# Kernel tuning notes

Measured on AMD Instinct MI355X. Metric: run time of the kernel, lower is better.

The kernel has to match this reference:

```python
import jax, jax.numpy as jnp
import numpy as np

N_NODES = 80000
N_EDGES = 1280000
D_NODE = 128
D_EDGE = 32
D_HID = 64
NEG_SLOPE = 0.2


def setup_inputs() -> dict:
    key = jax.random.key(0)
    ks = jax.random.split(key, 9)
    return {
        "node_features": jax.random.normal(ks[0], (N_NODES, D_NODE), dtype=jnp.float32),
        "edge_features": jax.random.normal(ks[1], (N_EDGES, D_EDGE), dtype=jnp.float32),
        "edge_index": jax.random.randint(ks[2], (2, N_EDGES), 0, N_NODES, dtype=jnp.int64),
        # params: w (node Linear), edgew (edge Linear), attn (3*hid -> 1)
        "w_w": jax.random.normal(ks[3], (D_NODE, D_HID), dtype=jnp.float32) / np.sqrt(D_NODE),
        "w_b": jax.random.normal(ks[4], (D_HID,), dtype=jnp.float32) * 0.01,
        "ew_w": jax.random.normal(ks[5], (D_EDGE, D_HID), dtype=jnp.float32) / np.sqrt(D_EDGE),
        "ew_b": jax.random.normal(ks[6], (D_HID,), dtype=jnp.float32) * 0.01,
        "a_w": jax.random.normal(ks[7], (3 * D_HID, 1), dtype=jnp.float32) / np.sqrt(3 * D_HID),
        "a_b": jax.random.normal(ks[8], (1,), dtype=jnp.float32) * 0.01,
    }


def reference(node_features, edge_features, edge_index, w_w, w_b, ew_w, ew_b, a_w, a_b):
    n_nodes = node_features.shape[0]
    h = node_features @ w_w + w_b              # [N, H]
    edge_h = edge_features @ ew_w + ew_b       # [E, H]
    tgt = edge_index[0]                        # target (softmax group) nodes i
    nbr = edge_index[1]                        # neighbor nodes j
    h_i = h[tgt]                               # [E, H] gather
    h_j = h[nbr]                               # [E, H] gather
    h_concat = jnp.concatenate([h_i, h_j, edge_h], axis=-1)  # [E, 3H]
    eij = jax.nn.leaky_relu(h_concat @ a_w + a_b, negative_slope=NEG_SLOPE)  # [E, 1]
    # scatter-softmax over edges grouped by target node (numerically stable)
    seg_max = jax.ops.segment_max(eij, tgt, num_segments=n_nodes)            # [N, 1]
    ex = jnp.exp(eij - seg_max[tgt])
    seg_sum = jax.ops.segment_sum(ex, tgt, num_segments=n_nodes)             # [N, 1]
    alpha = ex / seg_sum[tgt]                                                # [E, 1]
    # (dropout omitted for deterministic reference)
    message = alpha * h_j                                                    # [E, H]
    out = jax.ops.segment_sum(message, tgt, num_segments=n_nodes)            # [N, H]
    return jax.nn.elu(out)
```

## Files before the change

kernel.cpp:

```cpp
#include <hip/hip_runtime.h>
#include <math.h>

#define N_NODES 80000
#define N_EDGES 1280000
#define D_NODE  128
#define D_EDGE  32
#define D_HID   64
#define NEG_SLOPE 0.2f
#define NB 313
#define CAP 4608
#define EB_BLK 512
#define EB_CHUNK 2048
#define EB_NCHUNK (N_EDGES / EB_CHUNK)

__device__ inline float waveReduceSum(float v) {
    #pragma unroll
    for (int o = 32; o > 0; o >>= 1) v += __shfl_xor(v, o);
    return v;
}
__device__ inline unsigned short f2bf(float f) {
    unsigned u = __float_as_uint(f);
    return (unsigned short)((u + 0x7FFF + ((u >> 16) & 1)) >> 16);
}
__device__ inline float bf2f(unsigned short v) {
    return __uint_as_float(((unsigned)v) << 16);
}

__global__ __launch_bounds__(256) void node_kernel(
        const float* __restrict__ nf, const float* __restrict__ w_w,
        const float* __restrict__ w_b, const float* __restrict__ a_w,
        unsigned short* __restrict__ hb, float* __restrict__ s1, float* __restrict__ s2) {
    __shared__ float Ws[D_HID * D_NODE];
    __shared__ float Xs[32][D_NODE];
    for (int i = threadIdx.x; i < D_NODE * D_HID; i += 256) {
        int k = i >> 6, d = i & 63;
        Ws[d * D_NODE + (((k >> 2) ^ (d & 7)) << 2) + (k & 3)] = w_w[i];
    }
    int lane = threadIdx.x & 63;
    int wv   = threadIdx.x >> 6;
    float wb = w_b[lane];
    float a1 = a_w[lane];
    float a2 = a_w[D_HID + lane];
    const float* wrow = &Ws[lane * D_NODE];
    const int nTiles = N_NODES / 32;
    for (int tile = blockIdx.x; tile < nTiles; tile += gridDim.x) {
        int n0 = tile * 32;
        __syncthreads();
        {
            const float4* src = (const float4*)(nf + (size_t)n0 * D_NODE);
            float4* dst = (float4*)&Xs[0][0];
            #pragma unroll
            for (int j = 0; j < 4; ++j)
                dst[threadIdx.x + 256 * j] = src[threadIdx.x + 256 * j];
        }
        __syncthreads();
        float acc[8] = {0.f, 0.f, 0.f, 0.f, 0.f, 0.f, 0.f, 0.f};
        const float* xs = &Xs[wv * 8][0];
        #pragma unroll 4
        for (int k4 = 0; k4 < 32; ++k4) {
            float4 w = *(const float4*)&wrow[(k4 ^ (lane & 7)) << 2];
            #pragma unroll
            for (int n = 0; n < 8; ++n) {
                float4 x = *(const float4*)&xs[n * D_NODE + (k4 << 2)];
                acc[n] += w.x * x.x + w.y * x.y + w.z * x.z + w.w * x.w;
            }
        }
        #pragma unroll
        for (int n = 0; n < 8; ++n) {
            int node = n0 + wv * 8 + n;
            float hv = acc[n] + wb;
            hb[(size_t)node * D_HID + lane] = f2bf(hv);
            float r1 = waveReduceSum(hv * a1);
            float r2 = waveReduceSum(hv * a2);
            if (lane == 0) { s1[node] = r1; s2[node] = r2; }
        }
    }
}

__global__ __launch_bounds__(EB_BLK) void edge_bin_kernel(
        const float* __restrict__ ef, const int* __restrict__ eidx,
        const float* __restrict__ s2v,
        const float* __restrict__ ew_w, const float* __restrict__ ew_b,
        const float* __restrict__ a_w, const float* __restrict__ a_b,
        int* __restrict__ bcnt, int2* __restrict__ binned) {
    __shared__ float cs[D_EDGE];
    __shared__ float bes;
    __shared__ int hist[NB], gbase[NB], rank[NB];
    __shared__ float sq [EB_CHUNK];
    __shared__ int   stg[EB_CHUNK];
    __shared__ int   snb[EB_CHUNK];
    int tid = threadIdx.x;
    if (tid < D_EDGE) {
        float s = 0.f;
        #pragma unroll
        for (int d = 0; d < D_HID; ++d) s += ew_w[tid * D_HID + d] * a_w[2 * D_HID + d];
        cs[tid] = s;
    } else if (tid == D_EDGE) {
        float s = 0.f;
        #pragma unroll
        for (int d = 0; d < D_HID; ++d) s += ew_b[d] * a_w[2 * D_HID + d];
        bes = s + a_b[0];
    }
    int qd = tid >> 2;
    int j  = tid & 3;
    for (int c = blockIdx.x; c < EB_NCHUNK; c += gridDim.x) {
        for (int i = tid; i < NB; i += EB_BLK) { hist[i] = 0; rank[i] = 0; }
        __syncthreads();
        int e0 = c * EB_CHUNK;
        #pragma unroll
        for (int k = 0; k < 4; ++k) {
            int idx = k * EB_BLK + tid;
            int e = e0 + idx;
            int tg = eidx[e];
            int nb = eidx[N_EDGES + e];
            stg[idx] = tg;
            snb[idx] = nb;
            sq [idx] = bes + s2v[nb];
            atomicAdd(&hist[tg >> 8], 1);
        }
        __syncthreads();
        #pragma unroll 2
        for (int rr = 0; rr < EB_CHUNK / 128; ++rr) {
            int idx = rr * 128 + qd;
            int e = e0 + idx;
            const float4* f4 = (const float4*)ef;
            float4 fa = f4[(size_t)e * 8 + j];
            float4 fb = f4[(size_t)e * 8 + 4 + j];
            const float4 c1 = *(const float4*)&cs[j * 4];
            const float4 c2 = *(const float4*)&cs[16 + j * 4];
            float p = fa.x * c1.x + fa.y * c1.y + fa.z * c1.z + fa.w * c1.w
                    + fb.x * c2.x + fb.y * c2.y + fb.z * c2.z + fb.w * c2.w;
            p += __shfl_xor(p, 1);
            p += __shfl_xor(p, 2);
            if (j == 0) sq[idx] += p;
        }
        __syncthreads();
        for (int i = tid; i < NB; i += EB_BLK) {
            int cc = hist[i];
            if (cc) gbase[i] = i * CAP + atomicAdd(&bcnt[i], cc);
        }
        __syncthreads();
        #pragma unroll
        for (int k = 0; k < 4; ++k) {
            int idx = k * EB_BLK + tid;
            int tg = stg[idx];
            int b  = tg >> 8;
            int r  = atomicAdd(&rank[b], 1);
            binned[gbase[b] + r] = make_int2(((tg & 255) << 17) | snb[idx],
                                             __float_as_int(sq[idx]));
        }
        __syncthreads();
    }
}

__global__ __launch_bounds__(512) void bucket_scan_kernel(
        const int* __restrict__ bcnt, int* __restrict__ bbase,
        int* __restrict__ node_off) {
    __shared__ int buf[512];
    int v = (threadIdx.x < NB) ? bcnt[threadIdx.x] : 0;
    buf[threadIdx.x] = v;
    __syncthreads();
    for (int ofs = 1; ofs < 512; ofs <<= 1) {
        int t = (threadIdx.x >= (unsigned)ofs) ? buf[threadIdx.x - ofs] : 0;
        __syncthreads();
        buf[threadIdx.x] += t;
        __syncthreads();
    }
    if (threadIdx.x < NB) bbase[threadIdx.x] = buf[threadIdx.x] - v;
    if (threadIdx.x == NB - 1) bbase[NB] = buf[threadIdx.x];
    if (threadIdx.x == 0) node_off[N_NODES] = N_EDGES;
}

__global__ __launch_bounds__(256) void bucket_csr_kernel(
        const int* __restrict__ bcnt, const int* __restrict__ bbase,
        const int2* __restrict__ binned, int* __restrict__ node_off,
        int2* __restrict__ pay2) {
    __shared__ int nhist[256], buf[256], ncur[256];
    int b = blockIdx.x;
    int in0  = b * CAP;
    int cnt  = bcnt[b];
    int out0 = bbase[b];
    nhist[threadIdx.x] = 0;
    __syncthreads();
    for (int i = threadIdx.x; i < cnt; i += 256)
        atomicAdd(&nhist[binned[in0 + i].x >> 17], 1);
    __syncthreads();
    int v = nhist[threadIdx.x];
    buf[threadIdx.x] = v;
    __syncthreads();
    for (int ofs = 1; ofs < 256; ofs <<= 1) {
        int t = (threadIdx.x >= (unsigned)ofs) ? buf[threadIdx.x - ofs] : 0;
        __syncthreads();
        buf[threadIdx.x] += t;
        __syncthreads();
    }
    int excl = buf[threadIdx.x] - v;
    int n = b * 256 + (int)threadIdx.x;
    if (n < N_NODES) node_off[n] = out0 + excl;
    ncur[threadIdx.x] = excl;
    __syncthreads();
    for (int i = threadIdx.x; i < cnt; i += 256) {
        int2 p = binned[in0 + i];
        int r = atomicAdd(&ncur[p.x >> 17], 1);
        pay2[out0 + r] = make_int2(p.x & 0x1FFFF, p.y);
    }
}

__global__ __launch_bounds__(256) void accum_kernel(
        const int* __restrict__ node_off, const int2* __restrict__ pay2,
        const float* __restrict__ s1, const unsigned short* __restrict__ hb,
        float* __restrict__ out) {
    __shared__ float exs[4][64];
    __shared__ int   nbs[4][64];
    int wv = threadIdx.x >> 6, lane = threadIdx.x & 63;
    int node = blockIdx.x * 4 + wv;
    if (node >= N_NODES) return;
    int base = node_off[node];
    int cnt  = node_off[node + 1] - base;
    if (cnt == 0) { out[(size_t)node * D_HID + lane] = 0.f; return; }
    float s1i = s1[node];
    float sumex = 0.f, acc = 0.f;
    for (int c0 = 0; c0 < cnt; c0 += 64) {
        int i = c0 + lane;
        int nc = min(64, cnt - c0);
        float exv = 0.f; int nb = 0;
        if (i < cnt) {
            int2 p = pay2[base + i];
            nb = p.x;
            float s = s1i + __int_as_float(p.y);
            s = (s > 0.f) ? s : NEG_SLOPE * s;
            exv = __expf(s);
        }
        sumex += exv;
        exs[wv][lane] = exv;
        nbs[wv][lane] = nb;
        for (int j = 0; j < nc; ++j) {
            acc += exs[wv][j] * bf2f(hb[(size_t)nbs[wv][j] * D_HID + lane]);
        }
    }
    sumex = waveReduceSum(sumex);
    float o = acc / sumex;
    out[(size_t)node * D_HID + lane] = (o > 0.f) ? o : (__expf(o) - 1.f);
}

extern "C" void kernel_launch(void* const* d_in, const int* in_sizes, int n_in,
                              void* d_out, int out_size, void* d_ws, size_t ws_size,
                              hipStream_t stream) {
    const float* nf   = (const float*)d_in[0];
    const float* ef   = (const float*)d_in[1];
    const int*   eidx = (const int*)d_in[2];
    const float* w_w  = (const float*)d_in[3];
    const float* w_b  = (const float*)d_in[4];
    const float* ew_w = (const float*)d_in[5];
    const float* ew_b = (const float*)d_in[6];
    const float* a_w  = (const float*)d_in[7];
    const float* a_b  = (const float*)d_in[8];
    float* out = (float*)d_out;

    char* ws = (char*)d_ws;
    size_t o = 0;
    auto alloc = [&](size_t bytes) -> void* {
        void* p = ws + o;
        o = (o + bytes + 255) & ~(size_t)255;
        return p;
    };
    unsigned short* hb  = (unsigned short*)alloc((size_t)N_NODES * D_HID * 2);
    float* s1       = (float*)alloc((size_t)N_NODES * 4);
    float* s2       = (float*)alloc((size_t)N_NODES * 4);
    int*   bcnt     = (int*)alloc((size_t)NB * 4);
    int*   bbase    = (int*)alloc((size_t)(NB + 1) * 4);
    int*   node_off = (int*)alloc((size_t)(N_NODES + 1) * 4);
    int2*  binned   = (int2*)alloc((size_t)NB * CAP * 8);
    int2*  pay2     = (int2*)alloc((size_t)N_EDGES * 8);

    hipMemsetAsync(bcnt, 0, (size_t)NB * 4, stream);

    node_kernel<<<1250, 256, 0, stream>>>(nf, w_w, w_b, a_w, hb, s1, s2);
    edge_bin_kernel<<<EB_NCHUNK, EB_BLK, 0, stream>>>(ef, eidx, s2, ew_w, ew_b, a_w, a_b, bcnt, binned);
    bucket_scan_kernel<<<1, 512, 0, stream>>>(bcnt, bbase, node_off);
    bucket_csr_kernel<<<NB, 256, 0, stream>>>(bcnt, bbase, binned, node_off, pay2);
    accum_kernel<<<(N_NODES + 3) / 4, 256, 0, stream>>>(node_off, pay2, s1, hb, out);
}
```

Measured before the change: 163.5 us.

## Pad bucket counters, shrink edge-bin blocks, and pair-vectorize bf16 gathers in accum

Pads the global per-bucket atomic counters to a 16-int stride so they no longer share cache lines under contention. The edge binning kernel now runs one 1024-edge chunk per 256-thread block with no grid-stride loop, and hoists the coefficient loads out of the loop. The accumulation kernel has each lane load two bf16 values as one 32-bit word, with the two half-waves handling alternate edges and combined by a shuffle, then writes float2 outputs. This cuts the number of gather instructions and raises occupancy, at the cost of more blocks and atomics and an extra cross-half reduction.

```diff
diff --git a/kernel.cpp b/kernel.cpp
--- a/kernel.cpp
+++ b/kernel.cpp
@@ -9,8 +9,9 @@
 #define NEG_SLOPE 0.2f
 #define NB 313
 #define CAP 4608
-#define EB_BLK 512
-#define EB_CHUNK 2048
+#define BCNT_STRIDE 16
+#define EB_BLK 256
+#define EB_CHUNK 1024
 #define EB_NCHUNK (N_EDGES / EB_CHUNK)
 
 __device__ inline float waveReduceSum(float v) {
@@ -101,55 +102,53 @@
         for (int d = 0; d < D_HID; ++d) s += ew_b[d] * a_w[2 * D_HID + d];
         bes = s + a_b[0];
     }
+    for (int i = tid; i < NB; i += EB_BLK) { hist[i] = 0; rank[i] = 0; }
+    __syncthreads();
+    int c = blockIdx.x;
+    int e0 = c * EB_CHUNK;
+    #pragma unroll
+    for (int k = 0; k < 4; ++k) {
+        int idx = k * EB_BLK + tid;
+        int e = e0 + idx;
+        int tg = eidx[e];
+        int nb = eidx[N_EDGES + e];
+        stg[idx] = tg;
+        snb[idx] = nb;
+        sq [idx] = bes + s2v[nb];
+        atomicAdd(&hist[tg >> 8], 1);
+    }
+    __syncthreads();
     int qd = tid >> 2;
     int j  = tid & 3;
-    for (int c = blockIdx.x; c < EB_NCHUNK; c += gridDim.x) {
-        for (int i = tid; i < NB; i += EB_BLK) { hist[i] = 0; rank[i] = 0; }
-        __syncthreads();
-        int e0 = c * EB_CHUNK;
-        #pragma unroll
-        for (int k = 0; k < 4; ++k) {
-            int idx = k * EB_BLK + tid;
-            int e = e0 + idx;
-            int tg = eidx[e];
-            int nb = eidx[N_EDGES + e];
-            stg[idx] = tg;
-            snb[idx] = nb;
-            sq [idx] = bes + s2v[nb];
-            atomicAdd(&hist[tg >> 8], 1);
-        }
-        __syncthreads();
-        #pragma unroll 2
-        for (int rr = 0; rr < EB_CHUNK / 128; ++rr) {
-            int idx = rr * 128 + qd;
-            int e = e0 + idx;
-            const float4* f4 = (const float4*)ef;
-            float4 fa = f4[(size_t)e * 8 + j];
-            float4 fb = f4[(size_t)e * 8 + 4 + j];
-            const float4 c1 = *(const float4*)&cs[j * 4];
-            const float4 c2 = *(const float4*)&cs[16 + j * 4];
-            float p = fa.x * c1.x + fa.y * c1.y + fa.z * c1.z + fa.w * c1.w
-                    + fb.x * c2.x + fb.y * c2.y + fb.z * c2.z + fb.w * c2.w;
-            p += __shfl_xor(p, 1);
-            p += __shfl_xor(p, 2);
-            if (j == 0) sq[idx] += p;
-        }
-        __syncthreads();
-        for (int i = tid; i < NB; i += EB_BLK) {
-            int cc = hist[i];
-            if (cc) gbase[i] = i * CAP + atomicAdd(&bcnt[i], cc);
-        }
-        __syncthreads();
-        #pragma unroll
-        for (int k = 0; k < 4; ++k) {
-            int idx = k * EB_BLK + tid;
-            int tg = stg[idx];
-            int b  = tg >> 8;
-            int r  = atomicAdd(&rank[b], 1);
-            binned[gbase[b] + r] = make_int2(((tg & 255) << 17) | snb[idx],
-                                             __float_as_int(sq[idx]));
-        }
-        __syncthreads();
+    const float4 c1 = *(const float4*)&cs[j * 4];
+    const float4 c2 = *(const float4*)&cs[16 + j * 4];
+    const float4* f4 = (const float4*)ef;
+    #pragma unroll 4
+    for (int rr = 0; rr < EB_CHUNK / 64; ++rr) {
+        int idx = rr * 64 + qd;
+        int e = e0 + idx;
+        float4 fa = f4[(size_t)e * 8 + j];
+        float4 fb = f4[(size_t)e * 8 + 4 + j];
+        float p = fa.x * c1.x + fa.y * c1.y + fa.z * c1.z + fa.w * c1.w
+                + fb.x * c2.x + fb.y * c2.y + fb.z * c2.z + fb.w * c2.w;
+        p += __shfl_xor(p, 1);
+        p += __shfl_xor(p, 2);
+        if (j == 0) sq[idx] += p;
+    }
+    __syncthreads();
+    for (int i = tid; i < NB; i += EB_BLK) {
+        int cc = hist[i];
+        if (cc) gbase[i] = i * CAP + atomicAdd(&bcnt[i * BCNT_STRIDE], cc);
+    }
+    __syncthreads();
+    #pragma unroll
+    for (int k = 0; k < 4; ++k) {
+        int idx = k * EB_BLK + tid;
+        int tg = stg[idx];
+        int b  = tg >> 8;
+        int r  = atomicAdd(&rank[b], 1);
+        binned[gbase[b] + r] = make_int2(((tg & 255) << 17) | snb[idx],
+                                         __float_as_int(sq[idx]));
     }
 }
 
@@ -157,7 +156,7 @@
         const int* __restrict__ bcnt, int* __restrict__ bbase,
         int* __restrict__ node_off) {
     __shared__ int buf[512];
-    int v = (threadIdx.x < NB) ? bcnt[threadIdx.x] : 0;
+    int v = (threadIdx.x < NB) ? bcnt[threadIdx.x * BCNT_STRIDE] : 0;
     buf[threadIdx.x] = v;
     __syncthreads();
     for (int ofs = 1; ofs < 512; ofs <<= 1) {
@@ -178,7 +177,7 @@
     __shared__ int nhist[256], buf[256], ncur[256];
     int b = blockIdx.x;
     int in0  = b * CAP;
-    int cnt  = bcnt[b];
+    int cnt  = bcnt[b * BCNT_STRIDE];
     int out0 = bbase[b];
     nhist[threadIdx.x] = 0;
     __syncthreads();
@@ -213,13 +212,18 @@
     __shared__ float exs[4][64];
     __shared__ int   nbs[4][64];
     int wv = threadIdx.x >> 6, lane = threadIdx.x & 63;
+    int half = lane >> 5;
+    int fp   = lane & 31;
     int node = blockIdx.x * 4 + wv;
     if (node >= N_NODES) return;
     int base = node_off[node];
     int cnt  = node_off[node + 1] - base;
-    if (cnt == 0) { out[(size_t)node * D_HID + lane] = 0.f; return; }
+    if (cnt == 0) {
+        if (half == 0) ((float2*)out)[(size_t)node * 32 + fp] = make_float2(0.f, 0.f);
+        return;
+    }
     float s1i = s1[node];
-    float sumex = 0.f, acc = 0.f;
+    float sumex = 0.f, acc0 = 0.f, acc1 = 0.f;
     for (int c0 = 0; c0 < cnt; c0 += 64) {
         int i = c0 + lane;
         int nc = min(64, cnt - c0);
@@ -234,13 +238,26 @@
         sumex += exv;
         exs[wv][lane] = exv;
         nbs[wv][lane] = nb;
-        for (int j = 0; j < nc; ++j) {
-            acc += exs[wv][j] * bf2f(hb[(size_t)nbs[wv][j] * D_HID + lane]);
-        }
-    }
+        for (int j = 0; j < nc; j += 2) {
+            int jj = j + half;
+            float w = 0.f; unsigned v = 0;
+            if (jj < nc) {
+                w = exs[wv][jj];
+                v = *(const unsigned*)&hb[(size_t)nbs[wv][jj] * D_HID + fp * 2];
+            }
+            acc0 += w * bf2f((unsigned short)(v & 0xFFFF));
+            acc1 += w * bf2f((unsigned short)(v >> 16));
+        }
+    }
+    acc0 += __shfl_xor(acc0, 32);
+    acc1 += __shfl_xor(acc1, 32);
     sumex = waveReduceSum(sumex);
-    float o = acc / sumex;
-    out[(size_t)node * D_HID + lane] = (o > 0.f) ? o : (__expf(o) - 1.f);
+    if (half == 0) {
+        float o0 = acc0 / sumex, o1 = acc1 / sumex;
+        o0 = (o0 > 0.f) ? o0 : (__expf(o0) - 1.f);
+        o1 = (o1 > 0.f) ? o1 : (__expf(o1) - 1.f);
+        ((float2*)out)[(size_t)node * 32 + fp] = make_float2(o0, o1);
+    }
 }
 
 extern "C" void kernel_launch(void* const* d_in, const int* in_sizes, int n_in,
@@ -267,13 +284,13 @@
     unsigned short* hb  = (unsigned short*)alloc((size_t)N_NODES * D_HID * 2);
     float* s1       = (float*)alloc((size_t)N_NODES * 4);
     float* s2       = (float*)alloc((size_t)N_NODES * 4);
-    int*   bcnt     = (int*)alloc((size_t)NB * 4);
+    int*   bcnt     = (int*)alloc((size_t)NB * BCNT_STRIDE * 4);
     int*   bbase    = (int*)alloc((size_t)(NB + 1) * 4);
     int*   node_off = (int*)alloc((size_t)(N_NODES + 1) * 4);
     int2*  binned   = (int2*)alloc((size_t)NB * CAP * 8);
     int2*  pay2     = (int2*)alloc((size_t)N_EDGES * 8);
 
-    hipMemsetAsync(bcnt, 0, (size_t)NB * 4, stream);
+    hipMemsetAsync(bcnt, 0, (size_t)NB * BCNT_STRIDE * 4, stream);
 
     node_kernel<<<1250, 256, 0, stream>>>(nf, w_w, w_b, a_w, hb, s1, s2);
     edge_bin_kernel<<<EB_NCHUNK, EB_BLK, 0, stream>>>(ef, eidx, s2, ew_w, ew_b, a_w, a_b, bcnt, binned);
```

Result: slower. 194.3 us (+18.8%).
